# Kernel optimization log

Hardware: AMD Instinct MI355X
Metric: run time of the kernel (lower is better)

## Reference

```python
import jax, jax.numpy as jnp
import numpy as np

N_NODES = 100000
N_EDGES = 3200000
LATENT_DIM = 64


def _spmm(rows, cols, vals, x, num_segments):
    # y[i] = sum_{e: rows[e]==i} vals[e] * x[cols[e]]  -- COO sparse @ dense
    contrib = vals[:, None] * x[cols]          # [E, D]
    return jax.ops.segment_sum(contrib, rows, num_segments=num_segments)


def setup_inputs() -> dict:
    key = jax.random.key(0)
    k1, k2, k3, k4, k5 = jax.random.split(key, 5)
    x = jax.random.normal(k1, (N_NODES, LATENT_DIM), dtype=jnp.float32)
    alpha_train = jax.random.uniform(k2, (N_NODES,), dtype=jnp.float32)
    edge_rows = jax.random.randint(k3, (N_EDGES,), 0, N_NODES, dtype=jnp.int32)
    edge_cols = jax.random.randint(k4, (N_EDGES,), 0, N_NODES, dtype=jnp.int32)
    edge_vals = jax.random.uniform(k5, (N_EDGES,), dtype=jnp.float32)
    return {
        "t": 0,
        "x": x,
        "alpha_train": alpha_train,
        "edge_rows": edge_rows,
        "edge_cols": edge_cols,
        "edge_vals": edge_vals,
    }


def reference(t, x, alpha_train, edge_rows, edge_cols, edge_vals):
    # alph = sigmoid(alpha).unsqueeze(1)
    alph = jax.nn.sigmoid(alpha_train)[:, None]          # [N, 1]
    ax = _spmm(edge_rows, edge_cols, edge_vals, x, N_NODES)   # first hop: g @ x
    ax = alph * _spmm(edge_rows, edge_cols, edge_vals, ax, N_NODES)  # gated second hop
    f = ax - x                                           # residual
    return f
```

## Files before the change

### kernel.cpp

```cpp
#include <hip/hip_runtime.h>

#define LATENT 64
#define SUB_SHIFT 7
#define SUB_ROWS 128
#define COLBITS 17
#define COL_MASK ((1 << COLBITS) - 1)
#define TILE 4096
#define NSUB_PAD 1024

__device__ __forceinline__ unsigned short f2bf(float f) {
    unsigned u = __float_as_uint(f);
    unsigned r = (u + 0x7FFFu + ((u >> 16) & 1u)) >> 16;
    return (unsigned short)r;
}

__global__ void __launch_bounds__(512) hist_kernel(const int* __restrict__ rows,
                                                   int* __restrict__ part, int E, int nsub) {
    __shared__ int h[NSUB_PAD];
    int t = threadIdx.x;
    int tb = blockIdx.x * TILE;
    for (int i = t; i < NSUB_PAD; i += 512) h[i] = 0;
    __syncthreads();
    #pragma unroll
    for (int k = 0; k < TILE / 512; ++k) {
        int e = tb + k * 512 + t;
        if (e < E) atomicAdd(&h[rows[e] >> SUB_SHIFT], 1);
    }
    __syncthreads();
    for (int i = t; i < nsub; i += 512) part[blockIdx.x * nsub + i] = h[i];
}

__global__ void __launch_bounds__(1024) scanparts_kernel(int* __restrict__ part,
                                                         int* __restrict__ tot,
                                                         int nsub, int ntiles) {
    __shared__ int sc[1024];
    int s = blockIdx.x;
    int t = threadIdx.x;
    int v = (t < ntiles) ? part[t * nsub + s] : 0;
    sc[t] = v;
    __syncthreads();
    for (int o = 1; o < 1024; o <<= 1) {
        int u = (t >= o) ? sc[t - o] : 0;
        __syncthreads();
        sc[t] += u;
        __syncthreads();
    }
    if (t < ntiles) part[t * nsub + s] = sc[t] - v;
    if (t == 1023) tot[s] = sc[1023];
}

__global__ void subscan_kernel(const int* __restrict__ tot_in, int* __restrict__ csr0,
                               int* __restrict__ tstart, int* __restrict__ stot, int nsub) {
    __shared__ int tot[NSUB_PAD];
    __shared__ int sc[256];
    int t = threadIdx.x;
    for (int i = t; i < NSUB_PAD; i += 256) tot[i] = (i < nsub) ? tot_in[i] : 0;
    __syncthreads();
    int c0 = tot[4 * t], c1 = tot[4 * t + 1], c2 = tot[4 * t + 2], c3 = tot[4 * t + 3];
    int csum = c0 + c1 + c2 + c3;
    sc[t] = csum;
    __syncthreads();
    for (int o = 1; o < 256; o <<= 1) {
        int u = (t >= o) ? sc[t - o] : 0;
        __syncthreads();
        sc[t] += u;
        __syncthreads();
    }
    int pre = sc[t] - csum;
    int s0 = 4 * t;
    if (s0 < nsub)     { csr0[s0] = pre;     stot[s0] = c0;     tstart[s0] = pre + 8 * s0; }
    pre += c0;
    if (s0 + 1 < nsub) { csr0[s0 + 1] = pre; stot[s0 + 1] = c1; tstart[s0 + 1] = pre + 8 * (s0 + 1); }
    pre += c1;
    if (s0 + 2 < nsub) { csr0[s0 + 2] = pre; stot[s0 + 2] = c2; tstart[s0 + 2] = pre + 8 * (s0 + 2); }
    pre += c2;
    if (s0 + 3 < nsub) { csr0[s0 + 3] = pre; stot[s0 + 3] = c3; tstart[s0 + 3] = pre + 8 * (s0 + 3); }
}

__global__ void __launch_bounds__(512) place_kernel(
        const int* __restrict__ rows, const int* __restrict__ cols,
        const float* __restrict__ vals, const int* __restrict__ part,
        const int* __restrict__ tstart, int2* __restrict__ tmp, int E, int nsub) {
    __shared__ int gbase[NSUB_PAD];
    __shared__ int cur[NSUB_PAD];
    int t = threadIdx.x;
    int tb = blockIdx.x * TILE;
    for (int i = t; i < nsub; i += 512)
        gbase[i] = part[blockIdx.x * nsub + i] + tstart[i];
    for (int i = t; i < NSUB_PAD; i += 512) cur[i] = 0;
    __syncthreads();
    #pragma unroll
    for (int k = 0; k < TILE / 512; ++k) {
        int e = tb + k * 512 + t;
        if (e < E) {
            int r = rows[e];
            int b = r >> SUB_SHIFT;
            int p = gbase[b] + atomicAdd(&cur[b], 1);
            tmp[p] = make_int2(cols[e] | ((r & (SUB_ROWS - 1)) << COLBITS),
                               __float_as_int(vals[e]));
        }
    }
}

__global__ void conv_bf16_kernel(const float* __restrict__ in,
                                 unsigned short* __restrict__ outb, long long n4) {
    long long i = (long long)blockIdx.x * blockDim.x + threadIdx.x;
    long long stride = (long long)gridDim.x * blockDim.x;
    for (; i < n4; i += stride) {
        float4 f = reinterpret_cast<const float4*>(in)[i];
        ushort4 o;
        o.x = f2bf(f.x); o.y = f2bf(f.y); o.z = f2bf(f.z); o.w = f2bf(f.w);
        reinterpret_cast<ushort4*>(outb)[i] = o;
    }
}

__global__ void __launch_bounds__(512) subsort_kernel(
        const int2* __restrict__ tmp, const int* __restrict__ tstart,
        const int* __restrict__ stot, const int* __restrict__ csr0,
        int2* __restrict__ oc, int2* __restrict__ spair, int N) {
    __shared__ int lcnt[SUB_ROWS], lpos[SUB_ROWS], lcur[SUB_ROWS];
    int s = blockIdx.x;
    int t = threadIdx.x;
    int beg = tstart[s], n = stot[s], c0 = csr0[s];
    if (t < SUB_ROWS) lcnt[t] = 0;
    __syncthreads();
    for (int i = t; i < n; i += blockDim.x)
        atomicAdd(&lcnt[(tmp[beg + i].x >> COLBITS) & (SUB_ROWS - 1)], 1);
    __syncthreads();
    if (t < SUB_ROWS) lpos[t] = lcnt[t];
    __syncthreads();
    for (int o = 1; o < SUB_ROWS; o <<= 1) {
        int u = (t < SUB_ROWS && t >= o) ? lpos[t - o] : 0;
        __syncthreads();
        if (t < SUB_ROWS) lpos[t] += u;
        __syncthreads();
    }
    if (t < SUB_ROWS) {
        int excl = lpos[t] - lcnt[t];
        lcur[t] = excl;
        int row = (s << SUB_SHIFT) + t;
        if (row < N) oc[row] = make_int2(c0 + excl, lcnt[t]);
    }
    __syncthreads();
    for (int i = t; i < n; i += blockDim.x) {
        int2 w = tmp[beg + i];
        int rl = (w.x >> COLBITS) & (SUB_ROWS - 1);
        int p = atomicAdd(&lcur[rl], 1);
        spair[c0 + p] = make_int2(w.x & COL_MASK, w.y);
    }
}


#define FMA8(G, V)                                                              \
    acc0 += (V) * __uint_as_float((G).x << 16);                                 \
    acc1 += (V) * __uint_as_float((G).x & 0xFFFF0000u);                         \
    acc2 += (V) * __uint_as_float((G).y << 16);                                 \
    acc3 += (V) * __uint_as_float((G).y & 0xFFFF0000u);                         \
    acc4 += (V) * __uint_as_float((G).z << 16);                                 \
    acc5 += (V) * __uint_as_float((G).z & 0xFFFF0000u);                         \
    acc6 += (V) * __uint_as_float((G).w << 16);                                 \
    acc7 += (V) * __uint_as_float((G).w & 0xFFFF0000u);

#define GATHER_CORE(TBL)                                                        \
    int el = lane >> 3;                                                         \
    int f  = lane & 7;                                                          \
    const uint4* tb4 = (const uint4*)(TBL);                                     \
    const int2* sp = spair + el;                        \
    float acc0 = 0.f, acc1 = 0.f, acc2 = 0.f, acc3 = 0.f;                       \
    float acc4 = 0.f, acc5 = 0.f, acc6 = 0.f, acc7 = 0.f;                       \
    for (; e + 32 <= end; e += 32) {                                            \
        int2 w0 = sp[e];      int2 w1 = sp[e + 8];                              \
        int2 w2 = sp[e + 16]; int2 w3 = sp[e + 24];                             \
        uint4 g0 = tb4[(unsigned)w0.x * 8u + (unsigned)f];                      \
        uint4 g1 = tb4[(unsigned)w1.x * 8u + (unsigned)f];                      \
        uint4 g2 = tb4[(unsigned)w2.x * 8u + (unsigned)f];                      \
        uint4 g3 = tb4[(unsigned)w3.x * 8u + (unsigned)f];                      \
        float v0 = __int_as_float(w0.y), v1 = __int_as_float(w1.y);             \
        float v2 = __int_as_float(w2.y), v3 = __int_as_float(w3.y);             \
        FMA8(g0, v0)                                                            \
        FMA8(g1, v1)                                                            \
        FMA8(g2, v2)                                                            \
        FMA8(g3, v3)                                                            \
    }                                                                           \
    for (; e + 8 <= end; e += 8) {                                              \
        int2 w_ = sp[e];                                                        \
        uint4 g_ = tb4[(unsigned)w_.x * 8u + (unsigned)f];                      \
        float v_ = __int_as_float(w_.y);                                        \
        FMA8(g_, v_)                                                            \
    }                                                                           \
    if (e < end) {                                                              \
        int ei = e + el;                                                        \
        int ci = ei < end ? ei : end - 1;                                       \
        int2 w_ = spair[ci];                                                    \
        uint4 g_ = tb4[(unsigned)w_.x * 8u + (unsigned)f];                      \
        float v_ = (ei < end) ? __int_as_float(w_.y) : 0.f;                     \
        FMA8(g_, v_)                                                            \
    }                                                                           \
    acc0 += __shfl_xor(acc0, 8); acc0 += __shfl_xor(acc0, 16); acc0 += __shfl_xor(acc0, 32); \
    acc1 += __shfl_xor(acc1, 8); acc1 += __shfl_xor(acc1, 16); acc1 += __shfl_xor(acc1, 32); \
    acc2 += __shfl_xor(acc2, 8); acc2 += __shfl_xor(acc2, 16); acc2 += __shfl_xor(acc2, 32); \
    acc3 += __shfl_xor(acc3, 8); acc3 += __shfl_xor(acc3, 16); acc3 += __shfl_xor(acc3, 32); \
    acc4 += __shfl_xor(acc4, 8); acc4 += __shfl_xor(acc4, 16); acc4 += __shfl_xor(acc4, 32); \
    acc5 += __shfl_xor(acc5, 8); acc5 += __shfl_xor(acc5, 16); acc5 += __shfl_xor(acc5, 32); \
    acc6 += __shfl_xor(acc6, 8); acc6 += __shfl_xor(acc6, 16); acc6 += __shfl_xor(acc6, 32); \
    acc7 += __shfl_xor(acc7, 8); acc7 += __shfl_xor(acc7, 16); acc7 += __shfl_xor(acc7, 32);

__global__ void __launch_bounds__(256) spmm_gather1_kernel(
        const int2* __restrict__ oc, const int2* __restrict__ spair,
        const unsigned short* __restrict__ xb, unsigned short* __restrict__ axb, int N) {
    int wid = blockIdx.x * (blockDim.x >> 6) + (threadIdx.x >> 6);
    int lane = threadIdx.x & 63;
    if (wid >= N) return;
    int2 o = oc[wid];
    int e = o.x, end = o.x + o.y;
    GATHER_CORE(xb)
    if (el == 0) {
        uint4 pk;
        pk.x = (unsigned)f2bf(acc0) | ((unsigned)f2bf(acc1) << 16);
        pk.y = (unsigned)f2bf(acc2) | ((unsigned)f2bf(acc3) << 16);
        pk.z = (unsigned)f2bf(acc4) | ((unsigned)f2bf(acc5) << 16);
        pk.w = (unsigned)f2bf(acc6) | ((unsigned)f2bf(acc7) << 16);
        ((uint4*)axb)[(size_t)wid * 8 + f] = pk;
    }
}

__global__ void __launch_bounds__(256) spmm_gather2_kernel(
        const int2* __restrict__ oc, const int2* __restrict__ spair,
        const unsigned short* __restrict__ axb, const float* __restrict__ alpha,
        const float* __restrict__ x, float* __restrict__ out, int N) {
    int wid = blockIdx.x * (blockDim.x >> 6) + (threadIdx.x >> 6);
    int lane = threadIdx.x & 63;
    if (wid >= N) return;
    int2 o = oc[wid];
    int e = o.x, end = o.x + o.y;
    GATHER_CORE(axb)
    if (el == 0) {
        float a = 1.0f / (1.0f + __expf(-alpha[wid]));
        float4 xv0 = ((const float4*)x)[(size_t)wid * 16 + 2 * f];
        float4 xv1 = ((const float4*)x)[(size_t)wid * 16 + 2 * f + 1];
        float4 ov0, ov1;
        ov0.x = a * acc0 - xv0.x;
        ov0.y = a * acc1 - xv0.y;
        ov0.z = a * acc2 - xv0.z;
        ov0.w = a * acc3 - xv0.w;
        ov1.x = a * acc4 - xv1.x;
        ov1.y = a * acc5 - xv1.y;
        ov1.z = a * acc6 - xv1.z;
        ov1.w = a * acc7 - xv1.w;
        ((float4*)out)[(size_t)wid * 16 + 2 * f] = ov0;
        ((float4*)out)[(size_t)wid * 16 + 2 * f + 1] = ov1;
    }
}

__global__ void spmm_atomic_kernel(const int* __restrict__ rows, const int* __restrict__ cols,
                                   const float* __restrict__ vals, const float* __restrict__ x,
                                   float* __restrict__ y, int E) {
    long long tid = (long long)blockIdx.x * blockDim.x + threadIdx.x;
    long long total = (long long)E * 16;
    long long stride = (long long)gridDim.x * blockDim.x;
    for (; tid < total; tid += stride) {
        int e = (int)(tid >> 4);
        int q = (int)(tid & 15);
        int r = rows[e];
        int c = cols[e];
        float v = vals[e];
        float4 xv = reinterpret_cast<const float4*>(x)[(size_t)c * 16 + q];
        float* yp = y + (size_t)r * LATENT + q * 4;
        atomicAdd(yp + 0, v * xv.x);
        atomicAdd(yp + 1, v * xv.y);
        atomicAdd(yp + 2, v * xv.z);
        atomicAdd(yp + 3, v * xv.w);
    }
}

__global__ void finalize_kernel(const float* __restrict__ alpha, const float* __restrict__ x,
                                float* __restrict__ out, int N) {
    long long tid = (long long)blockIdx.x * blockDim.x + threadIdx.x;
    long long total = (long long)N * 16;
    long long stride = (long long)gridDim.x * blockDim.x;
    for (; tid < total; tid += stride) {
        int i = (int)(tid >> 4);
        float a = 1.0f / (1.0f + __expf(-alpha[i]));
        float4 ov = reinterpret_cast<float4*>(out)[tid];
        float4 xv = reinterpret_cast<const float4*>(x)[tid];
        ov.x = a * ov.x - xv.x;
        ov.y = a * ov.y - xv.y;
        ov.z = a * ov.z - xv.z;
        ov.w = a * ov.w - xv.w;
        reinterpret_cast<float4*>(out)[tid] = ov;
    }
}


extern "C" void kernel_launch(void* const* d_in, const int* in_sizes, int n_in,
                              void* d_out, int out_size, void* d_ws, size_t ws_size,
                              hipStream_t stream) {
    const float* x     = (const float*)d_in[1];
    const float* alpha = (const float*)d_in[2];
    const int*   rows  = (const int*)d_in[3];
    const int*   cols  = (const int*)d_in[4];
    const float* vals  = (const float*)d_in[5];

    const int N = in_sizes[2];
    const int E = in_sizes[3];
    float* out = (float*)d_out;

    const int block = 256;
    const int nsub   = (N + SUB_ROWS - 1) >> SUB_SHIFT;
    const int ntiles = (E + TILE - 1) / TILE;

    auto align256 = [](size_t v) { return (v + 255) & ~(size_t)255; };

    size_t tmp_bytes  = ((size_t)E + 8 * (size_t)nsub) * sizeof(int2);
    size_t xbf_bytes  = (size_t)N * LATENT * sizeof(unsigned short);
    size_t o_axbf_inA = align256(xbf_bytes);
    size_t bf_bytes   = o_axbf_inA + xbf_bytes;
    size_t RA = tmp_bytes > bf_bytes ? tmp_bytes : bf_bytes;

    size_t o_tmp    = 0;
    size_t o_spair  = align256(o_tmp + RA);
    size_t o_oc     = align256(o_spair + (size_t)E * sizeof(int2));
    size_t o_csr0   = align256(o_oc + (size_t)N * sizeof(int2));
    size_t o_tstart = align256(o_csr0 + (size_t)nsub * sizeof(int));
    size_t o_stot   = align256(o_tstart + (size_t)nsub * sizeof(int));
    size_t o_tot    = align256(o_stot + (size_t)nsub * sizeof(int));
    size_t needed   = o_tot + (size_t)nsub * sizeof(int);
    size_t part_bytes = (size_t)ntiles * nsub * sizeof(int);

    if (ws_size >= needed && nsub <= NSUB_PAD && N <= (1 << COLBITS) &&
        ntiles <= 1024 && part_bytes <= (size_t)E * sizeof(int2)) {
        char* ws = (char*)d_ws;
        int2*           tmp    = (int2*)(ws + o_tmp);
        unsigned short* xbf    = (unsigned short*)(ws + o_tmp);
        unsigned short* axbf   = (unsigned short*)(ws + o_tmp + o_axbf_inA);
        int2*           spair  = (int2*)(ws + o_spair);
        int*            part   = (int*)(ws + o_spair);
        int2*           oc     = (int2*)(ws + o_oc);
        int*            csr0   = (int*)(ws + o_csr0);
        int*            tstart = (int*)(ws + o_tstart);
        int*            stot   = (int*)(ws + o_stot);
        int*            tot    = (int*)(ws + o_tot);

        hist_kernel<<<ntiles, 512, 0, stream>>>(rows, part, E, nsub);
        scanparts_kernel<<<nsub, 1024, 0, stream>>>(part, tot, nsub, ntiles);
        subscan_kernel<<<1, 256, 0, stream>>>(tot, csr0, tstart, stot, nsub);
        place_kernel<<<ntiles, 512, 0, stream>>>(rows, cols, vals, part, tstart, tmp, E, nsub);
        subsort_kernel<<<nsub, 512, 0, stream>>>(tmp, tstart, stot, csr0, oc, spair, N);

        long long n4 = (long long)N * (LATENT / 4);
        conv_bf16_kernel<<<2048, 256, 0, stream>>>(x, xbf, n4);

        int rows_per_block = block / 64;
        int grid_rows = (N + rows_per_block - 1) / rows_per_block;
        spmm_gather1_kernel<<<grid_rows, block, 0, stream>>>(oc, spair, xbf, axbf, N);
        spmm_gather2_kernel<<<grid_rows, block, 0, stream>>>(oc, spair, axbf,
                                                             alpha, x, out, N);
        return;
    }

    {
        float* ax1 = (float*)d_ws;
        const size_t feat_bytes = (size_t)N * LATENT * sizeof(float);
        hipMemsetAsync(ax1, 0, feat_bytes, stream);
        hipMemsetAsync(out, 0, feat_bytes, stream);
        long long work = (long long)E * 16;
        int grid_spmm = (int)((work + block - 1) / block);
        spmm_atomic_kernel<<<grid_spmm, block, 0, stream>>>(rows, cols, vals, x, ax1, E);
        spmm_atomic_kernel<<<grid_spmm, block, 0, stream>>>(rows, cols, vals, ax1, out, E);
        long long fwork = (long long)N * 16;
        int grid_fin = (int)((fwork + block - 1) / block);
        finalize_kernel<<<grid_fin, block, 0, stream>>>(alpha, x, out, N);
    }
}
```

Before: 215.2 us.

## Stage place-kernel scatter in shared memory for coalesced bucket writes

The place kernel now does a local exclusive scan of each tile's bucket counts and scatters edges into a shared-memory staging buffer in bucket order. It then writes the buffer out contiguously, finding each element's bucket by binary search, so global writes become mostly contiguous runs instead of random scattered 8-byte stores. The tile size doubles to 8192 and the number of tiles halves, which shrinks the scanparts pass to 512 threads. The cost is 64KB+ of shared memory per block (lower occupancy), extra scans and binary searches, and a separate prefix buffer so the raw counts are preserved.

```diff
diff --git a/kernel.cpp b/kernel.cpp
--- a/kernel.cpp
+++ b/kernel.cpp
@@ -5,7 +5,7 @@
 #define SUB_ROWS 128
 #define COLBITS 17
 #define COL_MASK ((1 << COLBITS) - 1)
-#define TILE 4096
+#define TILE 8192
 #define NSUB_PAD 1024
 
 __device__ __forceinline__ unsigned short f2bf(float f) {
@@ -30,23 +30,24 @@
     for (int i = t; i < nsub; i += 512) part[blockIdx.x * nsub + i] = h[i];
 }
 
-__global__ void __launch_bounds__(1024) scanparts_kernel(int* __restrict__ part,
-                                                         int* __restrict__ tot,
-                                                         int nsub, int ntiles) {
-    __shared__ int sc[1024];
+__global__ void __launch_bounds__(512) scanparts_kernel(const int* __restrict__ part,
+                                                        int* __restrict__ pfx,
+                                                        int* __restrict__ tot,
+                                                        int nsub, int ntiles) {
+    __shared__ int sc[512];
     int s = blockIdx.x;
     int t = threadIdx.x;
     int v = (t < ntiles) ? part[t * nsub + s] : 0;
     sc[t] = v;
     __syncthreads();
-    for (int o = 1; o < 1024; o <<= 1) {
+    for (int o = 1; o < 512; o <<= 1) {
         int u = (t >= o) ? sc[t - o] : 0;
         __syncthreads();
         sc[t] += u;
         __syncthreads();
     }
-    if (t < ntiles) part[t * nsub + s] = sc[t] - v;
-    if (t == 1023) tot[s] = sc[1023];
+    if (t < ntiles) pfx[t * nsub + s] = sc[t] - v;
+    if (t == 511) tot[s] = sc[511];
 }
 
 __global__ void subscan_kernel(const int* __restrict__ tot_in, int* __restrict__ csr0,
@@ -77,17 +78,39 @@
     if (s0 + 3 < nsub) { csr0[s0 + 3] = pre; stot[s0 + 3] = c3; tstart[s0 + 3] = pre + 8 * (s0 + 3); }
 }
 
-__global__ void __launch_bounds__(512) place_kernel(
+__global__ void __launch_bounds__(512, 2) place_kernel(
         const int* __restrict__ rows, const int* __restrict__ cols,
         const float* __restrict__ vals, const int* __restrict__ part,
-        const int* __restrict__ tstart, int2* __restrict__ tmp, int E, int nsub) {
+        const int* __restrict__ pfx, const int* __restrict__ tstart,
+        int2* __restrict__ tmp, int E, int nsub) {
+    __shared__ int base[NSUB_PAD];
     __shared__ int gbase[NSUB_PAD];
     __shared__ int cur[NSUB_PAD];
+    __shared__ int2 stage[TILE];
+    __shared__ int sc[512];
     int t = threadIdx.x;
     int tb = blockIdx.x * TILE;
+    int tilecnt = E - tb; if (tilecnt > TILE) tilecnt = TILE;
+
+    const int* pc = part + (size_t)blockIdx.x * nsub;
+    int c0 = (2 * t < nsub) ? pc[2 * t] : 0;
+    int c1 = (2 * t + 1 < nsub) ? pc[2 * t + 1] : 0;
+    int csum = c0 + c1;
+    sc[t] = csum;
+    __syncthreads();
+    for (int o = 1; o < 512; o <<= 1) {
+        int u = (t >= o) ? sc[t - o] : 0;
+        __syncthreads();
+        sc[t] += u;
+        __syncthreads();
+    }
+    int ex = sc[t] - csum;
+    base[2 * t] = ex;
+    base[2 * t + 1] = ex + c0;
+    __syncthreads();
+    for (int i = t; i < NSUB_PAD; i += 512) cur[i] = 0;
     for (int i = t; i < nsub; i += 512)
-        gbase[i] = part[blockIdx.x * nsub + i] + tstart[i];
-    for (int i = t; i < NSUB_PAD; i += 512) cur[i] = 0;
+        gbase[i] = tstart[i] + pfx[(size_t)blockIdx.x * nsub + i] - base[i];
     __syncthreads();
     #pragma unroll
     for (int k = 0; k < TILE / 512; ++k) {
@@ -95,10 +118,16 @@
         if (e < E) {
             int r = rows[e];
             int b = r >> SUB_SHIFT;
-            int p = gbase[b] + atomicAdd(&cur[b], 1);
-            tmp[p] = make_int2(cols[e] | ((r & (SUB_ROWS - 1)) << COLBITS),
-                               __float_as_int(vals[e]));
+            int pos = base[b] + atomicAdd(&cur[b], 1);
+            stage[pos] = make_int2(cols[e] | ((r & (SUB_ROWS - 1)) << COLBITS),
+                                   __float_as_int(vals[e]));
         }
+    }
+    __syncthreads();
+    for (int p = t; p < tilecnt; p += 512) {
+        int lo = 0, hi = nsub;
+        while (hi - lo > 1) { int mid = (lo + hi) >> 1; if (base[mid] <= p) lo = mid; else hi = mid; }
+        tmp[gbase[lo] + p] = stage[p];
     }
 }
 
@@ -328,13 +357,14 @@
     size_t part_bytes = (size_t)ntiles * nsub * sizeof(int);
 
     if (ws_size >= needed && nsub <= NSUB_PAD && N <= (1 << COLBITS) &&
-        ntiles <= 1024 && part_bytes <= (size_t)E * sizeof(int2)) {
+        ntiles <= 512 && 2 * part_bytes <= (size_t)E * sizeof(int2)) {
         char* ws = (char*)d_ws;
         int2*           tmp    = (int2*)(ws + o_tmp);
         unsigned short* xbf    = (unsigned short*)(ws + o_tmp);
         unsigned short* axbf   = (unsigned short*)(ws + o_tmp + o_axbf_inA);
         int2*           spair  = (int2*)(ws + o_spair);
         int*            part   = (int*)(ws + o_spair);
+        int*            pfx    = (int*)(ws + o_spair + part_bytes);
         int2*           oc     = (int2*)(ws + o_oc);
         int*            csr0   = (int*)(ws + o_csr0);
         int*            tstart = (int*)(ws + o_tstart);
@@ -342,9 +372,10 @@
         int*            tot    = (int*)(ws + o_tot);
 
         hist_kernel<<<ntiles, 512, 0, stream>>>(rows, part, E, nsub);
-        scanparts_kernel<<<nsub, 1024, 0, stream>>>(part, tot, nsub, ntiles);
+        scanparts_kernel<<<nsub, 512, 0, stream>>>(part, pfx, tot, nsub, ntiles);
         subscan_kernel<<<1, 256, 0, stream>>>(tot, csr0, tstart, stot, nsub);
-        place_kernel<<<ntiles, 512, 0, stream>>>(rows, cols, vals, part, tstart, tmp, E, nsub);
+        place_kernel<<<ntiles, 512, 0, stream>>>(rows, cols, vals, part, pfx, tstart,
+                                                 tmp, E, nsub);
         subsort_kernel<<<nsub, 512, 0, stream>>>(tmp, tstart, stot, csr0, oc, spair, N);
 
         long long n4 = (long long)N * (LATENT / 4);
```

After: 197.0 us (median of 2 runs). 8.5% less time.
